# Kernel tuning notes

Hardware: AMD Instinct MI355X
Metric: run time of the kernel (lower is better)

Reference implementation:

```python
import jax, jax.numpy as jnp
import numpy as np

NQ, M, ND, N, H, DIM = 32, 32, 200, 160, 768, 128
TEMP = 0.1      # log_softmax temperature
TAU = 0.5       # gumbel-softmax temperature
NEG = -10000.0


def _l2norm(x):
    # F.normalize(p=2, dim=-1) with eps clamp
    n = jnp.maximum(jnp.linalg.norm(x, axis=-1, keepdims=True), 1e-12)
    return x / n


def setup_inputs() -> dict:
    key = jax.random.key(0)
    k1, k2, k3, k4, k5, k6 = jax.random.split(key, 6)
    Q = jax.random.normal(k1, (NQ, M, H), dtype=jnp.float32)
    D = jax.random.normal(k2, (ND, N, H), dtype=jnp.float32)
    q_mask = jax.random.randint(k3, (NQ, M), 0, 2).astype(jnp.float32)
    d_mask = jax.random.randint(k4, (ND, N), 0, 2).astype(jnp.float32)
    # pre-sampled Gumbel(0,1) noise for gumbel_softmax (fixed for determinism)
    u = jax.random.uniform(k5, (NQ, ND, M, N), dtype=jnp.float32,
                           minval=1e-6, maxval=1.0 - 1e-6)
    gumbel_noise = -jnp.log(-jnp.log(u))
    # proj_linear: Linear(768, dim, bias=False)
    W_proj = jax.random.normal(k6, (H, DIM), dtype=jnp.float32) / np.sqrt(H)
    return {"Q": Q, "D": D, "q_mask": q_mask, "d_mask": d_mask,
            "gumbel_noise": gumbel_noise, "W_proj": W_proj}


def reference(Q, D, q_mask, d_mask, gumbel_noise, W_proj):
    # project + L2-normalize token embeddings
    Qp = _l2norm(Q @ W_proj)            # [q, m, dim]
    Dp = _l2norm(D @ W_proj)            # [d, n, dim]

    # pairwise token similarities: [q, d, m, n]
    sim = jnp.einsum('qmh,dnh->qdmn', Qp, Dp)

    dm = d_mask[None, :, None, :]       # [1, d, 1, n]
    sim_masked = sim * dm + (1.0 - dm) * NEG

    logits = jax.nn.log_softmax(sim_masked / TEMP, axis=-1)

    # gumbel_softmax(tau=0.5, hard=True) with straight-through
    y_soft = jax.nn.softmax((logits + gumbel_noise) / TAU, axis=-1)
    idx = jnp.argmax(y_soft, axis=-1)
    y_hard = jax.nn.one_hot(idx, N, dtype=y_soft.dtype)
    y = jax.lax.stop_gradient(y_hard - y_soft) + y_soft

    # select doc token per query token, mask query tokens, sum -> [q, d]
    scores = (y * sim_masked).sum(-1)          # [q, d, m]
    scores = scores * q_mask[:, None, :]
    return scores.sum(-1)                      # [q, d]
```

## Files before the change

kernel.cpp:

```cpp
#include <hip/hip_runtime.h>
#include <math.h>

#define NQ_   32
#define M_    32
#define ND_   200
#define N_    160
#define H_    768
#define DIM_  128
#define DROWS_ (ND_ * N_)
#define QROWS_ (NQ_ * M_)
#define TROWS_ (DROWS_ + QROWS_)

__device__ __forceinline__ void gl_lds16(const float* g, float* l) {
    __builtin_amdgcn_global_load_lds(
        (const __attribute__((address_space(1))) unsigned int*)g,
        (__attribute__((address_space(3))) unsigned int*)l, 16, 0, 0);
}

__global__ __launch_bounds__(128) void proj_kernel(
    const float* __restrict__ Dmat, const float* __restrict__ Qmat,
    const float* __restrict__ W, float* __restrict__ DpT,
    float* __restrict__ QpT)
{
    __shared__ __align__(16) float Xt[16][16];
    __shared__ __align__(16) float Ws[16][128];
    const int tid  = threadIdx.x;
    const int lane = tid & 63;
    const int wv   = tid >> 6;
    const int rb   = blockIdx.x * 16;
    const int cg   = tid & 15;
    const int rg   = tid >> 4;
    const int xrow = lane >> 2;
    const int xc4  = lane & 3;

    const int rX = rb + xrow;
    const float* xr_ptr = (rX < DROWS_) ? (Dmat + (size_t)rX * H_)
                                        : (Qmat + (size_t)(rX - DROWS_) * H_);

    float acc[2][8];
#pragma unroll
    for (int i = 0; i < 2; ++i)
#pragma unroll
        for (int j = 0; j < 8; ++j) acc[i][j] = 0.0f;

    for (int kc = 0; kc < H_; kc += 16) {
        if (wv == 0) {
            float4 v = *reinterpret_cast<const float4*>(xr_ptr + kc + xc4 * 4);
            Xt[xc4*4+0][xrow] = v.x;
            Xt[xc4*4+1][xrow] = v.y;
            Xt[xc4*4+2][xrow] = v.z;
            Xt[xc4*4+3][xrow] = v.w;
        } else {
            const float* wsrc = W + (size_t)kc * DIM_;
#pragma unroll
            for (int t = 0; t < 8; ++t)
                gl_lds16(wsrc + t * 256 + lane * 4, &Ws[0][0] + t * 256);
        }
        __syncthreads();
#pragma unroll
        for (int k = 0; k < 16; ++k) {
            float a[2], b[8];
            *reinterpret_cast<float2*>(&a[0]) = *reinterpret_cast<const float2*>(&Xt[k][rg*2]);
            *reinterpret_cast<float4*>(&b[0]) = *reinterpret_cast<const float4*>(&Ws[k][cg*8]);
            *reinterpret_cast<float4*>(&b[4]) = *reinterpret_cast<const float4*>(&Ws[k][cg*8+4]);
#pragma unroll
            for (int i = 0; i < 2; ++i)
#pragma unroll
                for (int j = 0; j < 8; ++j)
                    acc[i][j] = fmaf(a[i], b[j], acc[i][j]);
        }
        __syncthreads();
    }

    float nrm[2];
#pragma unroll
    for (int i = 0; i < 2; ++i) {
        float ss = 0.0f;
#pragma unroll
        for (int j = 0; j < 8; ++j) ss = __fadd_rn(ss, __fmul_rn(acc[i][j], acc[i][j]));
        ss = __fadd_rn(ss, __shfl_xor(ss, 1));
        ss = __fadd_rn(ss, __shfl_xor(ss, 2));
        ss = __fadd_rn(ss, __shfl_xor(ss, 4));
        ss = __fadd_rn(ss, __shfl_xor(ss, 8));
        nrm[i] = fmaxf(sqrtf(ss), 1e-12f);
    }

    if (rb < DROWS_) {
        const int dd = rb / 160, n0 = rb - dd * 160;
        float* o = DpT + (size_t)dd * (DIM_ * N_) + n0 + rg * 2;
#pragma unroll
        for (int j = 0; j < 8; ++j) {
            float2 v;
            v.x = acc[0][j] / nrm[0];
            v.y = acc[1][j] / nrm[1];
            *reinterpret_cast<float2*>(o + (size_t)(cg*8 + j) * N_) = v;
        }
    } else {
        const int rq = rb - DROWS_;
        const int qq = rq >> 5, m0 = rq & 31;
        float* o = QpT + (size_t)qq * (DIM_ * M_) + m0 + rg * 2;
#pragma unroll
        for (int j = 0; j < 8; ++j) {
            float2 v;
            v.x = acc[0][j] / nrm[0];
            v.y = acc[1][j] / nrm[1];
            *reinterpret_cast<float2*>(o + (size_t)(cg*8 + j) * M_) = v;
        }
    }
}

__global__ __launch_bounds__(64) void score_kernel(
    const float* __restrict__ QpT, const float* __restrict__ DpT,
    const float* __restrict__ qmask, const float* __restrict__ dmask,
    const float* __restrict__ gum, float* __restrict__ out)
{
    __shared__ float Qt[8][32];
    __shared__ float Dt[8][160];
    const int lane = threadIdx.x;
    const int mg   = lane >> 4;
    const int ng   = lane & 15;
    const int q    = blockIdx.x & 31;
    const int d    = blockIdx.x >> 5;

    const float* Qb = QpT + (size_t)q * (DIM_ * M_);
    const float* Db = DpT + (size_t)d * (DIM_ * N_);

    float acc[8][10];
#pragma unroll
    for (int i = 0; i < 8; ++i)
#pragma unroll
        for (int j = 0; j < 10; ++j) acc[i][j] = 0.0f;

    for (int kc = 0; kc < DIM_; kc += 8) {
        gl_lds16(Qb + kc * M_ + lane * 4, &Qt[0][0]);
#pragma unroll
        for (int c = 0; c < 5; ++c)
            gl_lds16(Db + kc * N_ + c * 256 + lane * 4, &Dt[0][0] + c * 256);
        __syncthreads();
#pragma unroll
        for (int k = 0; k < 8; ++k) {
            float a[8], b[10];
            *reinterpret_cast<float4*>(&a[0]) = *reinterpret_cast<const float4*>(&Qt[k][mg*8]);
            *reinterpret_cast<float4*>(&a[4]) = *reinterpret_cast<const float4*>(&Qt[k][mg*8+4]);
            const float* bp = &Dt[k][ng*10];
#pragma unroll
            for (int j2 = 0; j2 < 5; ++j2)
                *reinterpret_cast<float2*>(&b[j2*2]) = *reinterpret_cast<const float2*>(&bp[j2*2]);
#pragma unroll
            for (int i = 0; i < 8; ++i)
#pragma unroll
                for (int j = 0; j < 10; ++j)
                    acc[i][j] = fmaf(a[i], b[j], acc[i][j]);
        }
        __syncthreads();
    }

    float dmv[10];
#pragma unroll
    for (int j = 0; j < 10; ++j)
        dmv[j] = dmask[(size_t)d * N_ + ng*10 + j];

    const float* gq = gum + ((size_t)q * ND_ + d) * ((size_t)M_ * N_);

    float partial = 0.0f;
#pragma unroll
    for (int i = 0; i < 8; ++i) {
        const int m = mg*8 + i;
        float x[10];
        float mx = -3.402823466e38f;
#pragma unroll
        for (int j = 0; j < 10; ++j) {
            float sm = (dmv[j] != 0.0f) ? acc[i][j] : -10000.0f;
            x[j] = sm / 0.1f;
            mx = fmaxf(mx, x[j]);
        }
        mx = fmaxf(mx, __shfl_xor(mx, 1));
        mx = fmaxf(mx, __shfl_xor(mx, 2));
        mx = fmaxf(mx, __shfl_xor(mx, 4));
        mx = fmaxf(mx, __shfl_xor(mx, 8));

        float se = 0.0f;
#pragma unroll
        for (int j = 0; j < 10; ++j) se = __fadd_rn(se, expf(x[j] - mx));
        se = __fadd_rn(se, __shfl_xor(se, 1));
        se = __fadd_rn(se, __shfl_xor(se, 2));
        se = __fadd_rn(se, __shfl_xor(se, 4));
        se = __fadd_rn(se, __shfl_xor(se, 8));
        const float lse = logf(se);

        float g[10];
        const float2* gp = reinterpret_cast<const float2*>(&gq[(size_t)m * N_ + ng*10]);
#pragma unroll
        for (int j2 = 0; j2 < 5; ++j2)
            *reinterpret_cast<float2*>(&g[j2*2]) = gp[j2];

        float z[10];
        float mz = -3.402823466e38f;
#pragma unroll
        for (int j = 0; j < 10; ++j) {
            z[j] = ((x[j] - mx - lse) + g[j]) / 0.5f;
            mz = fmaxf(mz, z[j]);
        }
        mz = fmaxf(mz, __shfl_xor(mz, 1));
        mz = fmaxf(mz, __shfl_xor(mz, 2));
        mz = fmaxf(mz, __shfl_xor(mz, 4));
        mz = fmaxf(mz, __shfl_xor(mz, 8));

        float e2[10];
        float s2 = 0.0f;
#pragma unroll
        for (int j = 0; j < 10; ++j) { e2[j] = expf(z[j] - mz); s2 = __fadd_rn(s2, e2[j]); }
        s2 = __fadd_rn(s2, __shfl_xor(s2, 1));
        s2 = __fadd_rn(s2, __shfl_xor(s2, 2));
        s2 = __fadd_rn(s2, __shfl_xor(s2, 4));
        s2 = __fadd_rn(s2, __shfl_xor(s2, 8));

        float besty = -1.0f; int bestn = 0x7fffffff; float bests = 0.0f;
#pragma unroll
        for (int j = 0; j < 10; ++j) {
            float y = e2[j] / s2;
            if (y > besty) {
                besty = y;
                bestn = ng*10 + j;
                bests = (dmv[j] != 0.0f) ? acc[i][j] : -10000.0f;
            }
        }
#pragma unroll
        for (int dl = 1; dl < 16; dl <<= 1) {
            float oy = __shfl_xor(besty, dl);
            int   on = __shfl_xor(bestn, dl);
            float os = __shfl_xor(bests, dl);
            if (oy > besty || (oy == besty && on < bestn)) {
                besty = oy; bestn = on; bests = os;
            }
        }
        const float qmv = qmask[q * M_ + m];
        if (ng == 0) partial = __fadd_rn(partial, __fmul_rn(bests, qmv));
    }
    partial = __fadd_rn(partial, __shfl_xor(partial, 16));
    partial = __fadd_rn(partial, __shfl_xor(partial, 32));
    if (lane == 0) out[(size_t)q * ND_ + d] = partial;
}

extern "C" void kernel_launch(void* const* d_in, const int* in_sizes, int n_in,
                              void* d_out, int out_size, void* d_ws, size_t ws_size,
                              hipStream_t stream)
{
    const float* Q   = (const float*)d_in[0];
    const float* D   = (const float*)d_in[1];
    const float* qm  = (const float*)d_in[2];
    const float* dm  = (const float*)d_in[3];
    const float* gum = (const float*)d_in[4];
    const float* W   = (const float*)d_in[5];
    float* out = (float*)d_out;

    float* QpT = (float*)d_ws;
    float* DpT = QpT + (size_t)QROWS_ * DIM_;

    proj_kernel<<<dim3(TROWS_ / 16), dim3(128), 0, stream>>>(D, Q, W, DpT, QpT);
    score_kernel<<<dim3(NQ_ * ND_), dim3(64), 0, stream>>>(QpT, DpT, qm, dm, gum, out);
}
```

Before: 517.3 us.

## Double-buffer proj kernel in a single wave; pack two waves per score block

The projection kernel now runs one 64-lane wave per block instead of two. Each lane computes a 4x8 tile rather than 2x8. W and X chunks are double-buffered in LDS, and __syncthreads is replaced by explicit vmcnt/lgkmcnt waits, so the next chunk's global loads overlap the current chunk's FMAs. The score kernel places two independent (q,d) jobs per 128-thread block, each wave with its own LDS tiles, and drops block barriers in favour of per-wave waitcnts. This relies on single-wave ordering for LDS hazards, and the larger proj accumulator raises register pressure.

```diff
diff --git a/kernel.cpp b/kernel.cpp
--- a/kernel.cpp
+++ b/kernel.cpp
@@ -17,19 +17,20 @@
         (__attribute__((address_space(3))) unsigned int*)l, 16, 0, 0);
 }
 
-__global__ __launch_bounds__(128) void proj_kernel(
+#define ASM_VMCNT0 asm volatile("s_waitcnt vmcnt(0)" ::: "memory")
+#define ASM_LGKM0  asm volatile("s_waitcnt lgkmcnt(0)" ::: "memory")
+
+__global__ __launch_bounds__(64) void proj_kernel(
     const float* __restrict__ Dmat, const float* __restrict__ Qmat,
     const float* __restrict__ W, float* __restrict__ DpT,
     float* __restrict__ QpT)
 {
-    __shared__ __align__(16) float Xt[16][16];
-    __shared__ __align__(16) float Ws[16][128];
-    const int tid  = threadIdx.x;
-    const int lane = tid & 63;
-    const int wv   = tid >> 6;
+    __shared__ __align__(16) float Xt[2][16][16];
+    __shared__ __align__(16) float Ws[2][16][128];
+    const int lane = threadIdx.x;
     const int rb   = blockIdx.x * 16;
-    const int cg   = tid & 15;
-    const int rg   = tid >> 4;
+    const int cg   = lane & 15;
+    const int rg   = lane >> 4;
     const int xrow = lane >> 2;
     const int xc4  = lane & 3;
 
@@ -37,44 +38,52 @@
     const float* xr_ptr = (rX < DROWS_) ? (Dmat + (size_t)rX * H_)
                                         : (Qmat + (size_t)(rX - DROWS_) * H_);
 
-    float acc[2][8];
-#pragma unroll
-    for (int i = 0; i < 2; ++i)
+    float acc[4][8];
+#pragma unroll
+    for (int i = 0; i < 4; ++i)
 #pragma unroll
         for (int j = 0; j < 8; ++j) acc[i][j] = 0.0f;
 
-    for (int kc = 0; kc < H_; kc += 16) {
-        if (wv == 0) {
-            float4 v = *reinterpret_cast<const float4*>(xr_ptr + kc + xc4 * 4);
-            Xt[xc4*4+0][xrow] = v.x;
-            Xt[xc4*4+1][xrow] = v.y;
-            Xt[xc4*4+2][xrow] = v.z;
-            Xt[xc4*4+3][xrow] = v.w;
-        } else {
+#pragma unroll
+    for (int t = 0; t < 8; ++t)
+        gl_lds16(W + t * 256 + lane * 4, &Ws[0][0][0] + t * 256);
+    float4 xreg = *reinterpret_cast<const float4*>(xr_ptr + xc4 * 4);
+
+    for (int c = 0; c < 48; ++c) {
+        const int cb = c & 1;
+        Xt[cb][xc4*4+0][xrow] = xreg.x;
+        Xt[cb][xc4*4+1][xrow] = xreg.y;
+        Xt[cb][xc4*4+2][xrow] = xreg.z;
+        Xt[cb][xc4*4+3][xrow] = xreg.w;
+        ASM_VMCNT0;
+        ASM_LGKM0;
+        if (c < 47) {
+            const int kc = (c + 1) * 16;
             const float* wsrc = W + (size_t)kc * DIM_;
+            float* wdst = &Ws[cb ^ 1][0][0];
 #pragma unroll
             for (int t = 0; t < 8; ++t)
-                gl_lds16(wsrc + t * 256 + lane * 4, &Ws[0][0] + t * 256);
-        }
-        __syncthreads();
+                gl_lds16(wsrc + t * 256 + lane * 4, wdst + t * 256);
+            xreg = *reinterpret_cast<const float4*>(xr_ptr + kc + xc4 * 4);
+        }
+        __builtin_amdgcn_sched_barrier(0);
 #pragma unroll
         for (int k = 0; k < 16; ++k) {
-            float a[2], b[8];
-            *reinterpret_cast<float2*>(&a[0]) = *reinterpret_cast<const float2*>(&Xt[k][rg*2]);
-            *reinterpret_cast<float4*>(&b[0]) = *reinterpret_cast<const float4*>(&Ws[k][cg*8]);
-            *reinterpret_cast<float4*>(&b[4]) = *reinterpret_cast<const float4*>(&Ws[k][cg*8+4]);
-#pragma unroll
-            for (int i = 0; i < 2; ++i)
+            float a[4], b[8];
+            *reinterpret_cast<float4*>(&a[0]) = *reinterpret_cast<const float4*>(&Xt[cb][k][rg*4]);
+            *reinterpret_cast<float4*>(&b[0]) = *reinterpret_cast<const float4*>(&Ws[cb][k][cg*8]);
+            *reinterpret_cast<float4*>(&b[4]) = *reinterpret_cast<const float4*>(&Ws[cb][k][cg*8+4]);
+#pragma unroll
+            for (int i = 0; i < 4; ++i)
 #pragma unroll
                 for (int j = 0; j < 8; ++j)
                     acc[i][j] = fmaf(a[i], b[j], acc[i][j]);
         }
-        __syncthreads();
-    }
-
-    float nrm[2];
-#pragma unroll
-    for (int i = 0; i < 2; ++i) {
+    }
+
+    float nrm[4];
+#pragma unroll
+    for (int i = 0; i < 4; ++i) {
         float ss = 0.0f;
 #pragma unroll
         for (int j = 0; j < 8; ++j) ss = __fadd_rn(ss, __fmul_rn(acc[i][j], acc[i][j]));
@@ -87,43 +96,52 @@
 
     if (rb < DROWS_) {
         const int dd = rb / 160, n0 = rb - dd * 160;
-        float* o = DpT + (size_t)dd * (DIM_ * N_) + n0 + rg * 2;
+        float* o = DpT + (size_t)dd * (DIM_ * N_) + n0 + rg * 4;
 #pragma unroll
         for (int j = 0; j < 8; ++j) {
-            float2 v;
+            float4 v;
             v.x = acc[0][j] / nrm[0];
             v.y = acc[1][j] / nrm[1];
-            *reinterpret_cast<float2*>(o + (size_t)(cg*8 + j) * N_) = v;
+            v.z = acc[2][j] / nrm[2];
+            v.w = acc[3][j] / nrm[3];
+            *reinterpret_cast<float4*>(o + (size_t)(cg*8 + j) * N_) = v;
         }
     } else {
         const int rq = rb - DROWS_;
         const int qq = rq >> 5, m0 = rq & 31;
-        float* o = QpT + (size_t)qq * (DIM_ * M_) + m0 + rg * 2;
+        float* o = QpT + (size_t)qq * (DIM_ * M_) + m0 + rg * 4;
 #pragma unroll
         for (int j = 0; j < 8; ++j) {
-            float2 v;
+            float4 v;
             v.x = acc[0][j] / nrm[0];
             v.y = acc[1][j] / nrm[1];
-            *reinterpret_cast<float2*>(o + (size_t)(cg*8 + j) * M_) = v;
-        }
-    }
-}
-
-__global__ __launch_bounds__(64) void score_kernel(
+            v.z = acc[2][j] / nrm[2];
+            v.w = acc[3][j] / nrm[3];
+            *reinterpret_cast<float4*>(o + (size_t)(cg*8 + j) * M_) = v;
+        }
+    }
+}
+
+__global__ __launch_bounds__(128) void score_kernel(
     const float* __restrict__ QpT, const float* __restrict__ DpT,
     const float* __restrict__ qmask, const float* __restrict__ dmask,
     const float* __restrict__ gum, float* __restrict__ out)
 {
-    __shared__ float Qt[8][32];
-    __shared__ float Dt[8][160];
-    const int lane = threadIdx.x;
+    __shared__ float Qt[2][8][32];
+    __shared__ float Dt[2][8][160];
+    const int tid  = threadIdx.x;
+    const int lane = tid & 63;
+    const int wv   = tid >> 6;
     const int mg   = lane >> 4;
     const int ng   = lane & 15;
-    const int q    = blockIdx.x & 31;
-    const int d    = blockIdx.x >> 5;
+    const int job  = blockIdx.x * 2 + wv;
+    const int q    = job & 31;
+    const int d    = job >> 5;
 
     const float* Qb = QpT + (size_t)q * (DIM_ * M_);
     const float* Db = DpT + (size_t)d * (DIM_ * N_);
+    float* qt = &Qt[wv][0][0];
+    float* dt = &Dt[wv][0][0];
 
     float acc[8][10];
 #pragma unroll
@@ -132,17 +150,19 @@
         for (int j = 0; j < 10; ++j) acc[i][j] = 0.0f;
 
     for (int kc = 0; kc < DIM_; kc += 8) {
-        gl_lds16(Qb + kc * M_ + lane * 4, &Qt[0][0]);
+        ASM_LGKM0;
+        gl_lds16(Qb + kc * M_ + lane * 4, qt);
 #pragma unroll
         for (int c = 0; c < 5; ++c)
-            gl_lds16(Db + kc * N_ + c * 256 + lane * 4, &Dt[0][0] + c * 256);
-        __syncthreads();
+            gl_lds16(Db + kc * N_ + c * 256 + lane * 4, dt + c * 256);
+        ASM_VMCNT0;
+        __builtin_amdgcn_sched_barrier(0);
 #pragma unroll
         for (int k = 0; k < 8; ++k) {
             float a[8], b[10];
-            *reinterpret_cast<float4*>(&a[0]) = *reinterpret_cast<const float4*>(&Qt[k][mg*8]);
-            *reinterpret_cast<float4*>(&a[4]) = *reinterpret_cast<const float4*>(&Qt[k][mg*8+4]);
-            const float* bp = &Dt[k][ng*10];
+            *reinterpret_cast<float4*>(&a[0]) = *reinterpret_cast<const float4*>(qt + k*32 + mg*8);
+            *reinterpret_cast<float4*>(&a[4]) = *reinterpret_cast<const float4*>(qt + k*32 + mg*8 + 4);
+            const float* bp = dt + k*160 + ng*10;
 #pragma unroll
             for (int j2 = 0; j2 < 5; ++j2)
                 *reinterpret_cast<float2*>(&b[j2*2]) = *reinterpret_cast<const float2*>(&bp[j2*2]);
@@ -152,7 +172,6 @@
                 for (int j = 0; j < 10; ++j)
                     acc[i][j] = fmaf(a[i], b[j], acc[i][j]);
         }
-        __syncthreads();
     }
 
     float dmv[10];
@@ -257,6 +276,6 @@
     float* QpT = (float*)d_ws;
     float* DpT = QpT + (size_t)QROWS_ * DIM_;
 
-    proj_kernel<<<dim3(TROWS_ / 16), dim3(128), 0, stream>>>(D, Q, W, DpT, QpT);
-    score_kernel<<<dim3(NQ_ * ND_), dim3(64), 0, stream>>>(QpT, DpT, qm, dm, gum, out);
-}
+    proj_kernel<<<dim3(TROWS_ / 16), dim3(64), 0, stream>>>(D, Q, W, DpT, QpT);
+    score_kernel<<<dim3(NQ_ * ND_ / 2), dim3(128), 0, stream>>>(QpT, DpT, qm, dm, gum, out);
+}
```

New measurement: 533.1 us. +3.1%, slower.
